# Performance work log

Measured on AMD Instinct MI355X. Metric: run time of the kernel, lower is better.

The kernel has to match this reference:

```python
import jax, jax.numpy as jnp
import numpy as np

DIM = 4096
N_HEADS = 32
HEAD_DIM = DIM // N_HEADS
N_TOKENS = 8192


def setup_inputs() -> dict:
    key = jax.random.key(0)
    kx, kq, kk, kv, ko = jax.random.split(key, 5)
    # weights scaled ~N(0, 0.02) so softmax is not fully saturated (original uses torch.rand init,
    # but init distribution is irrelevant to the op's math)
    scale = 0.02
    return {
        "x": jax.random.normal(kx, (N_TOKENS, DIM), dtype=jnp.float32),
        "W_q": jax.random.normal(kq, (DIM, DIM), dtype=jnp.float32) * scale,
        "W_k": jax.random.normal(kk, (DIM, DIM), dtype=jnp.float32) * scale,
        "W_v": jax.random.normal(kv, (DIM, DIM), dtype=jnp.float32) * scale,
        "W_o": jax.random.normal(ko, (DIM, DIM), dtype=jnp.float32) * scale,
    }


def reference(x, W_q, W_k, W_v, W_o):
    # x: [N, dim]
    N = x.shape[0]
    Q = (x @ W_q).reshape(N, N_HEADS, HEAD_DIM)  # [N, h, d]
    K = (x @ W_k).reshape(N, N_HEADS, HEAD_DIM)
    V = (x @ W_v).reshape(N, N_HEADS, HEAD_DIM)
    # Faithful to the source: batched matmul over the token axis N, giving a
    # per-token [h, h] head-mixing matrix (NOT sequence attention). No 1/sqrt(d) scaling.
    scores = jnp.einsum("nhd,ngd->nhg", Q, K)          # [N, h, h]
    attn = jax.nn.softmax(scores, axis=2)
    y = jnp.einsum("nhg,ngd->nhd", attn, V)              # [N, h, d]
    return y.reshape(N, DIM) @ W_o
```

## Files before the change

### kernel.cpp

```cpp
#include <hip/hip_runtime.h>

#define DIM   4096
#define NTOK  8192
#define NH    32
#define HD    128

typedef _Float16 f16x8 __attribute__((ext_vector_type(8)));
typedef float    f32x4 __attribute__((ext_vector_type(4)));

__device__ __forceinline__ unsigned short f2h(float f) {
    _Float16 h = (_Float16)f;
    return __builtin_bit_cast(unsigned short, h);
}
__device__ __forceinline__ float h2f(unsigned short u) {
    return (float)__builtin_bit_cast(_Float16, u);
}

__device__ __forceinline__ void async_ld16(const unsigned short* g, unsigned short* l) {
    __builtin_amdgcn_global_load_lds(
        (const __attribute__((address_space(1))) unsigned int*)g,
        (__attribute__((address_space(3))) unsigned int*)l,
        16, 0, 0);
}

__global__ __launch_bounds__(256)
void convert_x(const float* __restrict__ in, unsigned short* __restrict__ out) {
    const size_t i = ((size_t)blockIdx.x * 256 + threadIdx.x) * 8;
    float4 a = *(const float4*)(in + i);
    float4 b = *(const float4*)(in + i + 4);
    ushort4 o0 = { f2h(a.x), f2h(a.y), f2h(a.z), f2h(a.w) };
    ushort4 o1 = { f2h(b.x), f2h(b.y), f2h(b.z), f2h(b.w) };
    *(ushort4*)(out + i)     = o0;
    *(ushort4*)(out + i + 4) = o1;
}

__global__ __launch_bounds__(256)
void transpose_cvt4k(const float* __restrict__ in, unsigned short* __restrict__ out) {
    __shared__ unsigned short tile[32][33];
    const int tx = threadIdx.x & 31;
    const int ty = threadIdx.x >> 5;
    const int n0 = blockIdx.x * 32;
    const int k0 = blockIdx.y * 32;
#pragma unroll
    for (int i = 0; i < 4; ++i)
        tile[ty + i * 8][tx] = f2h(in[(size_t)(k0 + ty + i * 8) * DIM + n0 + tx]);
    __syncthreads();
#pragma unroll
    for (int i = 0; i < 4; ++i)
        out[(size_t)(n0 + ty + i * 8) * DIM + k0 + tx] = tile[tx][ty + i * 8];
}

#define BARRIER() do { __builtin_amdgcn_sched_barrier(0); \
                       __builtin_amdgcn_s_barrier();      \
                       __builtin_amdgcn_sched_barrier(0); } while (0)
#define VMCNT6()  asm volatile("s_waitcnt vmcnt(6)" ::: "memory")

template <int Q>
__device__ __forceinline__ void mfma_quad(f32x4 (&acc)[8][4],
                                          const f16x8 (&aQ)[2][2],
                                          const f16x8 (&bF)[4][2]) {
    __builtin_amdgcn_s_setprio(1);
#pragma unroll
    for (int i2 = 0; i2 < 2; ++i2)
#pragma unroll
        for (int j = 0; j < 4; ++j)
#pragma unroll
            for (int ks = 0; ks < 2; ++ks)
                acc[2 * Q + i2][j] = __builtin_amdgcn_mfma_f32_16x16x32_f16(
                    aQ[i2][ks], bF[j][ks], acc[2 * Q + i2][j], 0, 0, 0);
    __builtin_amdgcn_s_setprio(0);
}

template <int OUT_F16>
__global__ __launch_bounds__(512, 2)
void gemm_nt_256(const unsigned short* __restrict__ A,
                 const unsigned short* __restrict__ Bt,
                 void* __restrict__ C, int M, int N, int K) {
    __shared__ unsigned short sA[2 * 256 * 64];
    __shared__ unsigned short sB[2 * 256 * 64];

    const int nwg = gridDim.x;
    const int bid = blockIdx.x;
    const int wg  = (bid & 7) * (nwg >> 3) + (bid >> 3);
    const int nbx = N >> 8;
    const int m0  = (wg / nbx) * 256;
    const int n0  = (wg % nbx) * 256;

    const int t    = threadIdx.x;
    const int w    = t >> 6;
    const int lane = t & 63;
    const int wm   = w >> 2;
    const int wn   = w & 3;
    const int fr   = lane & 15;
    const int kq   = (lane >> 4) << 3;
    const int swz  = (fr & 7) << 3;
    const int c0   = kq ^ swz;
    const int c1   = (32 + kq) ^ swz;

    const int rowt = t >> 3;
    const int cSw8 = ((t & 7) ^ (rowt & 7)) << 3;
    const unsigned short* gA = A  + (size_t)(m0 + rowt) * K + cSw8;
    const unsigned short* gB = Bt + (size_t)(n0 + rowt) * K + cSw8;
    unsigned short* dA = sA + w * 512;
    unsigned short* dB = sB + w * 512;
    const unsigned short* pA0 = sA + (wm * 128 + fr) * 64;
    const unsigned short* pB0 = sB + (wn * 64  + fr) * 64;

    const int KT = K >> 6;

    f32x4 acc[8][4];
#pragma unroll
    for (int i = 0; i < 8; ++i)
#pragma unroll
        for (int j = 0; j < 4; ++j) acc[i][j] = (f32x4){0.f, 0.f, 0.f, 0.f};
    f16x8 aQ[2][2], bF[4][2];

#define STA(srcT, dpar, r0) async_ld16(gA + (size_t)(r0) * K + (size_t)(srcT) * 64, \
                                       dA + (dpar) * 16384 + (r0) * 64)
#define STB(srcT, dpar, r0) async_ld16(gB + (size_t)(r0) * K + (size_t)(srcT) * 64, \
                                       dB + (dpar) * 16384 + (r0) * 64)
#define LDF(p, off) (*(const f16x8*)(const void*)((p) + (off)))

    STA(0, 0, 0); STA(0, 0, 64); STA(0, 0, 128); STA(0, 0, 192);
    STB(0, 0, 0); STB(0, 0, 64); STB(0, 0, 128); STB(0, 0, 192);
    STB(1, 1, 0); STB(1, 1, 64); STB(1, 1, 128); STB(1, 1, 192);
    STA(1, 1, 0); STA(1, 1, 128);
    VMCNT6();
    BARRIER();

#define KTILE(T, BUF) do {                                                        \
    const int T1c = ((T) + 1 < KT) ? (T) + 1 : KT - 1;   \
    const int T2c = ((T) + 2 < KT) ? (T) + 2 : KT - 1;                            \
    const unsigned short* pa = pA0 + (BUF) * 16384;                               \
    const unsigned short* pb = pB0 + (BUF) * 16384;                               \
                             \
    bF[0][0] = LDF(pb,        c0); bF[0][1] = LDF(pb,        c1);                 \
    bF[1][0] = LDF(pb, 1024 + c0); bF[1][1] = LDF(pb, 1024 + c1);                 \
    bF[2][0] = LDF(pb, 2048 + c0); bF[2][1] = LDF(pb, 2048 + c1);                 \
    bF[3][0] = LDF(pb, 3072 + c0); bF[3][1] = LDF(pb, 3072 + c1);                 \
    aQ[0][0] = LDF(pa,        c0); aQ[0][1] = LDF(pa,        c1);                 \
    aQ[1][0] = LDF(pa, 1024 + c0); aQ[1][1] = LDF(pa, 1024 + c1);                 \
    STA(T1c, (BUF) ^ 1, 64); STA(T1c, (BUF) ^ 1, 192);                            \
    BARRIER(); mfma_quad<0>(acc, aQ, bF); BARRIER();                              \
                                                                          \
    aQ[0][0] = LDF(pa, 2048 + c0); aQ[0][1] = LDF(pa, 2048 + c1);                 \
    aQ[1][0] = LDF(pa, 3072 + c0); aQ[1][1] = LDF(pa, 3072 + c1);                 \
    STB(T2c, (BUF), 0); STB(T2c, (BUF), 64);                                      \
    BARRIER(); mfma_quad<1>(acc, aQ, bF); BARRIER();                              \
                                                                          \
    aQ[0][0] = LDF(pa, 4096 + c0); aQ[0][1] = LDF(pa, 4096 + c1);                 \
    aQ[1][0] = LDF(pa, 5120 + c0); aQ[1][1] = LDF(pa, 5120 + c1);                 \
    STB(T2c, (BUF), 128); STB(T2c, (BUF), 192);                                   \
    BARRIER(); mfma_quad<2>(acc, aQ, bF); BARRIER();                              \
                                  \
    aQ[0][0] = LDF(pa, 6144 + c0); aQ[0][1] = LDF(pa, 6144 + c1);                 \
    aQ[1][0] = LDF(pa, 7168 + c0); aQ[1][1] = LDF(pa, 7168 + c1);                 \
    STA(T2c, (BUF), 0); STA(T2c, (BUF), 128);                                     \
    BARRIER(); mfma_quad<3>(acc, aQ, bF); VMCNT6(); BARRIER();                    \
} while (0)

    for (int it = 0; it < (KT >> 1); ++it) {
        const int kt = it << 1;
        KTILE(kt, 0);
        KTILE(kt + 1, 1);
    }
#undef KTILE
#undef STA
#undef STB
#undef LDF

    const int col0 = n0 + wn * 64 + fr;
    const int row0 = m0 + wm * 128 + (lane >> 4) * 4;
#pragma unroll
    for (int i = 0; i < 8; ++i) {
#pragma unroll
        for (int r = 0; r < 4; ++r) {
            const size_t row = (size_t)(row0 + i * 16 + r);
#pragma unroll
            for (int j = 0; j < 4; ++j) {
                const size_t idx = row * (size_t)N + (size_t)(col0 + j * 16);
                if (OUT_F16) ((unsigned short*)C)[idx] = f2h(acc[i][j][r]);
                else         ((float*)C)[idx]          = acc[i][j][r];
            }
        }
    }
}

__global__ __launch_bounds__(256)
void attn_kernel(const float* __restrict__ Q, const float* __restrict__ K,
                 const unsigned short* __restrict__ V, unsigned short* __restrict__ Y) {
    __shared__ float sQ[NH * HD];
    __shared__ float sK[NH * HD];
    __shared__ unsigned short sV[NH * HD];
    __shared__ float sS[NH * 33];

    const int n = blockIdx.x;
    const int t = threadIdx.x;
    const size_t base = (size_t)n * DIM;

    const float4* gQ = (const float4*)(Q + base);
    const float4* gK = (const float4*)(K + base);
#pragma unroll
    for (int i = 0; i < 4; ++i) {
        const int f = t + 256 * i;
        const int r = f >> 5;
        const int p = (f & 31) ^ ((r >> 1) & 7);
        ((float4*)sQ)[r * 32 + p] = gQ[f];
        ((float4*)sK)[r * 32 + p] = gK[f];
    }
    const float4* gV = (const float4*)(V + base);
#pragma unroll
    for (int i = 0; i < 2; ++i)
        ((float4*)sV)[t + 256 * i] = gV[t + 256 * i];
    __syncthreads();

    {
        const int th = (t >> 4) * 2;
        const int tg = (t & 15) * 2;
        const int sq = (th >> 1) & 7;
        const int sk = (tg >> 1) & 7;
        float s00 = 0.f, s01 = 0.f, s10 = 0.f, s11 = 0.f;
        const float4* q0 = (const float4*)(sQ + th * HD);
        const float4* q1 = (const float4*)(sQ + (th + 1) * HD);
        const float4* k0 = (const float4*)(sK + tg * HD);
        const float4* k1 = (const float4*)(sK + (tg + 1) * HD);
#pragma unroll 4
        for (int d = 0; d < HD / 4; ++d) {
            float4 a0 = q0[d ^ sq], a1 = q1[d ^ sq];
            float4 b0 = k0[d ^ sk], b1 = k1[d ^ sk];
            s00 += a0.x * b0.x + a0.y * b0.y + a0.z * b0.z + a0.w * b0.w;
            s01 += a0.x * b1.x + a0.y * b1.y + a0.z * b1.z + a0.w * b1.w;
            s10 += a1.x * b0.x + a1.y * b0.y + a1.z * b0.z + a1.w * b0.w;
            s11 += a1.x * b1.x + a1.y * b1.y + a1.z * b1.z + a1.w * b1.w;
        }
        sS[th * 33 + tg] = s00;       sS[th * 33 + tg + 1] = s01;
        sS[(th + 1) * 33 + tg] = s10; sS[(th + 1) * 33 + tg + 1] = s11;
    }
    __syncthreads();

    if (t < NH) {
        float m = -1e30f;
        for (int g = 0; g < NH; ++g) m = fmaxf(m, sS[t * 33 + g]);
        float sum = 0.f;
        for (int g = 0; g < NH; ++g) { float e = __expf(sS[t * 33 + g] - m); sS[t * 33 + g] = e; sum += e; }
        float inv = 1.f / sum;
        for (int g = 0; g < NH; ++g) sS[t * 33 + g] *= inv;
    }
    __syncthreads();

#pragma unroll
    for (int e = 0; e < 2; ++e) {
        const int task = t + e * 256;
        const int h0 = (task >> 5) * 2;
        const int dg = (task & 31) * 4;
        float a0x = 0, a0y = 0, a0z = 0, a0w = 0;
        float a1x = 0, a1y = 0, a1z = 0, a1w = 0;
#pragma unroll 4
        for (int g = 0; g < NH; ++g) {
            ushort4 uv = *(const ushort4*)(const void*)(sV + g * HD + dg);
            float vx = h2f(uv.x), vy = h2f(uv.y), vz = h2f(uv.z), vw = h2f(uv.w);
            float p0 = sS[h0 * 33 + g], p1 = sS[(h0 + 1) * 33 + g];
            a0x += p0 * vx; a0y += p0 * vy; a0z += p0 * vz; a0w += p0 * vw;
            a1x += p1 * vx; a1y += p1 * vy; a1z += p1 * vz; a1w += p1 * vw;
        }
        ushort4 o0 = { f2h(a0x), f2h(a0y), f2h(a0z), f2h(a0w) };
        ushort4 o1 = { f2h(a1x), f2h(a1y), f2h(a1z), f2h(a1w) };
        *(ushort4*)(void*)(Y + base + (size_t)h0 * HD + dg)       = o0;
        *(ushort4*)(void*)(Y + base + (size_t)(h0 + 1) * HD + dg) = o1;
    }
}

extern "C" void kernel_launch(void* const* d_in, const int* in_sizes, int n_in,
                              void* d_out, int out_size, void* d_ws, size_t ws_size,
                              hipStream_t stream) {
    const float* x  = (const float*)d_in[0];
    const float* Wq = (const float*)d_in[1];
    const float* Wk = (const float*)d_in[2];
    const float* Wv = (const float*)d_in[3];
    const float* Wo = (const float*)d_in[4];
    float* out = (float*)d_out;

    const size_t WT = (size_t)DIM * DIM * 2;
    const size_t XB = (size_t)NTOK * DIM * 2;
    const size_t QF = (size_t)NTOK * DIM * 4;
    const size_t VB = (size_t)NTOK * DIM * 2;
    const size_t NEED = WT + XB + 2 * QF + VB;
    if (ws_size < NEED) return;

    char* ws = (char*)d_ws;
    unsigned short* Wt = (unsigned short*)ws;
    unsigned short* xh = (unsigned short*)(ws + WT);
    float*          Qf = (float*)(ws + WT + XB);
    float*          Kf = (float*)(ws + WT + XB + QF);
    unsigned short* Vh = (unsigned short*)(ws + WT + XB + 2 * QF);
    unsigned short* Yh = xh;

    dim3 tgrid(DIM / 32, DIM / 32);
    const int ggrid = (NTOK / 256) * (DIM / 256);
    const int cblocks = (NTOK * DIM) / (256 * 8);

    convert_x<<<cblocks, 256, 0, stream>>>(x, xh);
    transpose_cvt4k<<<tgrid, 256, 0, stream>>>(Wq, Wt);
    gemm_nt_256<0><<<ggrid, 512, 0, stream>>>(xh, Wt, Qf, NTOK, DIM, DIM);
    transpose_cvt4k<<<tgrid, 256, 0, stream>>>(Wk, Wt);
    gemm_nt_256<0><<<ggrid, 512, 0, stream>>>(xh, Wt, Kf, NTOK, DIM, DIM);
    transpose_cvt4k<<<tgrid, 256, 0, stream>>>(Wv, Wt);
    gemm_nt_256<1><<<ggrid, 512, 0, stream>>>(xh, Wt, Vh, NTOK, DIM, DIM);
    attn_kernel<<<NTOK, 256, 0, stream>>>(Qf, Kf, Vh, Yh);
    transpose_cvt4k<<<tgrid, 256, 0, stream>>>(Wo, Wt);
    gemm_nt_256<0><<<ggrid, 512, 0, stream>>>(Yh, Wt, out, NTOK, DIM, DIM);
}
```

Before: 1.530 ms.

## Double-buffer A fragments and cut barriers in GEMM K-tile loop

Splits the A-fragment registers into two alternating sets so LDS reads for the next quad can be issued while the current MFMA quad executes. The per-quad barrier pairs are removed, leaving fewer barriers per K-tile, and the four B prefetch loads are grouped after a single barrier. This targets barrier stalls and LDS-to-MFMA latency. In exchange it uses more VGPRs and relies on the reordered barriers still guarding the LDS buffer overwrites against in-flight reads.

```diff
diff --git a/kernel.cpp b/kernel.cpp
--- a/kernel.cpp
+++ b/kernel.cpp
@@ -113,7 +113,7 @@
     for (int i = 0; i < 8; ++i)
 #pragma unroll
         for (int j = 0; j < 4; ++j) acc[i][j] = (f32x4){0.f, 0.f, 0.f, 0.f};
-    f16x8 aQ[2][2], bF[4][2];
+    f16x8 aA[2][2], aB[2][2], bF[4][2];
 
 #define STA(srcT, dpar, r0) async_ld16(gA + (size_t)(r0) * K + (size_t)(srcT) * 64, \
                                        dA + (dpar) * 16384 + (r0) * 64)
@@ -133,30 +133,34 @@
     const int T2c = ((T) + 2 < KT) ? (T) + 2 : KT - 1;                            \
     const unsigned short* pa = pA0 + (BUF) * 16384;                               \
     const unsigned short* pb = pB0 + (BUF) * 16384;                               \
-                             \
+         \
     bF[0][0] = LDF(pb,        c0); bF[0][1] = LDF(pb,        c1);                 \
     bF[1][0] = LDF(pb, 1024 + c0); bF[1][1] = LDF(pb, 1024 + c1);                 \
     bF[2][0] = LDF(pb, 2048 + c0); bF[2][1] = LDF(pb, 2048 + c1);                 \
     bF[3][0] = LDF(pb, 3072 + c0); bF[3][1] = LDF(pb, 3072 + c1);                 \
-    aQ[0][0] = LDF(pa,        c0); aQ[0][1] = LDF(pa,        c1);                 \
-    aQ[1][0] = LDF(pa, 1024 + c0); aQ[1][1] = LDF(pa, 1024 + c1);                 \
+    aA[0][0] = LDF(pa,        c0); aA[0][1] = LDF(pa,        c1);                 \
+    aA[1][0] = LDF(pa, 1024 + c0); aA[1][1] = LDF(pa, 1024 + c1);                 \
     STA(T1c, (BUF) ^ 1, 64); STA(T1c, (BUF) ^ 1, 192);                            \
-    BARRIER(); mfma_quad<0>(acc, aQ, bF); BARRIER();                              \
-                                                                          \
-    aQ[0][0] = LDF(pa, 2048 + c0); aQ[0][1] = LDF(pa, 2048 + c1);                 \
-    aQ[1][0] = LDF(pa, 3072 + c0); aQ[1][1] = LDF(pa, 3072 + c1);                 \
-    STB(T2c, (BUF), 0); STB(T2c, (BUF), 64);                                      \
-    BARRIER(); mfma_quad<1>(acc, aQ, bF); BARRIER();                              \
-                                                                          \
-    aQ[0][0] = LDF(pa, 4096 + c0); aQ[0][1] = LDF(pa, 4096 + c1);                 \
-    aQ[1][0] = LDF(pa, 5120 + c0); aQ[1][1] = LDF(pa, 5120 + c1);                 \
+    mfma_quad<0>(acc, aA, bF);                                                    \
+                                        \
+    aB[0][0] = LDF(pa, 2048 + c0); aB[0][1] = LDF(pa, 2048 + c1);                 \
+    aB[1][0] = LDF(pa, 3072 + c0); aB[1][1] = LDF(pa, 3072 + c1);                 \
+    BARRIER();         \
+    STB(T2c, (BUF), 0);   STB(T2c, (BUF), 64);                                    \
     STB(T2c, (BUF), 128); STB(T2c, (BUF), 192);                                   \
-    BARRIER(); mfma_quad<2>(acc, aQ, bF); BARRIER();                              \
-                                  \
-    aQ[0][0] = LDF(pa, 6144 + c0); aQ[0][1] = LDF(pa, 6144 + c1);                 \
-    aQ[1][0] = LDF(pa, 7168 + c0); aQ[1][1] = LDF(pa, 7168 + c1);                 \
+    mfma_quad<1>(acc, aB, bF);                                                    \
+                                        \
+    aA[0][0] = LDF(pa, 4096 + c0); aA[0][1] = LDF(pa, 4096 + c1);                 \
+    aA[1][0] = LDF(pa, 5120 + c0); aA[1][1] = LDF(pa, 5120 + c1);                 \
+    BARRIER();   \
     STA(T2c, (BUF), 0); STA(T2c, (BUF), 128);                                     \
-    BARRIER(); mfma_quad<3>(acc, aQ, bF); VMCNT6(); BARRIER();                    \
+    mfma_quad<2>(acc, aA, bF);                                                    \
+    \
+    aB[0][0] = LDF(pa, 6144 + c0); aB[0][1] = LDF(pa, 6144 + c1);                 \
+    aB[1][0] = LDF(pa, 7168 + c0); aB[1][1] = LDF(pa, 7168 + c1);                 \
+    mfma_quad<3>(acc, aB, bF);                                                    \
+    VMCNT6();                                                                     \
+    BARRIER();           \
 } while (0)
 
     for (int it = 0; it < (KT >> 1); ++it) {
```

Result: no change. 1.547 ms (+1.1%).
